# Kernel tuning notes

Measured on AMD Instinct MI355X. Metric: run time of the kernel, lower is better.

The kernel has to match this reference:

```python
import jax, jax.numpy as jnp
import numpy as np

N_NODES = 20000
N_EDGES = 320000
BATCH = 8
N_OBS = 6
N_FIXED = 10
HID = 128
N_LAYERS = 3


def setup_inputs() -> dict:
    key = jax.random.key(0)
    ks = jax.random.split(key, 6)
    x = jax.random.normal(ks[0], (BATCH * N_NODES, N_OBS), dtype=jnp.float32)
    fixed_node_features = jax.random.normal(ks[1], (N_NODES, N_FIXED), dtype=jnp.float32)
    edge_index = jax.random.randint(ks[2], (2, N_EDGES), 0, N_NODES)
    W_in = jax.random.normal(ks[3], (N_OBS + N_FIXED, HID), dtype=jnp.float32) * 0.1
    b_in = jnp.zeros((HID,), jnp.float32)
    Wg = jax.random.normal(ks[4], (N_LAYERS, HID, HID), dtype=jnp.float32) * 0.05
    bg = jnp.zeros((N_LAYERS, HID), jnp.float32)
    return {"x": x, "fixed_node_features": fixed_node_features, "W_in": W_in,
            "b_in": b_in, "Wg": Wg, "bg": bg, "edge_index": edge_index}


def reference(x, fixed_node_features, W_in, b_in, Wg, bg, edge_index):
    # GCN normalization with self-loops (PyG gcn_norm defaults):
    self_loops = jnp.arange(N_NODES)
    row = jnp.concatenate([edge_index[0], self_loops])  # source nodes [E+N]
    col = jnp.concatenate([edge_index[1], self_loops])  # target nodes [E+N]
    deg = jax.ops.segment_sum(jnp.ones_like(col, dtype=jnp.float32), col,
                              num_segments=N_NODES)
    dinv = jnp.where(deg > 0, jax.lax.rsqrt(jnp.maximum(deg, 1.0)), 0.0)
    norm = dinv[row] * dinv[col]  # [E+N]

    # input projection: [B*N, n_obs] -> [B, N, n_obs+n_fixed] -> [B, N, H]
    h = x.reshape(BATCH, N_NODES, N_OBS)
    h = jnp.concatenate(
        [h, jnp.broadcast_to(fixed_node_features, (BATCH, N_NODES, N_FIXED))],
        axis=-1)
    h = h @ W_in + b_in

    # stacked GCNConv + ReLU (gather -> normalize -> scatter-add)
    for l in range(N_LAYERS):
        t = h @ Wg[l]                              # [B, N, H]
        msgs = t[:, row, :] * norm[None, :, None]  # [B, E+N, H]
        agg = jnp.zeros_like(t).at[:, col, :].add(msgs)
        h = jax.nn.relu(agg + bg[l])

    return h.reshape(-1, HID)
```

## Files before the change

### kernel.cpp

```cpp
#include <hip/hip_runtime.h>
#include <hip/hip_bf16.h>
#include <cstdint>

#define N_NODES 20000
#define N_EDGES 320000
#define BATCH 8
#define HID 128

static constexpr size_t O_DEG  = 0;
static constexpr size_t O_CUR  = 81920;
static constexpr size_t O_OFF  = 163840;
static constexpr size_t O_DINV = 245760;
static constexpr size_t O_CSR  = 327680;
static constexpr size_t O_CSRW = 1376256;
static constexpr size_t O_HBUF = 3473408;


__global__ void count_deg(const int* __restrict__ col, int* __restrict__ deg) {
    int e = blockIdx.x * 256 + threadIdx.x;
    if (e < N_EDGES) atomicAdd(&deg[col[e]], 1);
}

__global__ void compute_dinv(const int* __restrict__ deg, float* __restrict__ dinv) {
    int i = blockIdx.x * 256 + threadIdx.x;
    if (i < N_NODES) {
        float d = (float)(deg[i] + 1);
        dinv[i] = 1.0f / sqrtf(d);
    }
}

__global__ __launch_bounds__(1024) void scan_offsets(const int* __restrict__ deg,
                                                     int* __restrict__ off) {
    __shared__ int part[1024];
    const int CH = 20;
    int tid = threadIdx.x;
    int base = tid * CH;
    int s = 0;
    for (int i = 0; i < CH; ++i) {
        int idx = base + i;
        if (idx < N_NODES) s += (deg[idx] + 7) & ~7;
    }
    part[tid] = s;
    __syncthreads();
    for (int d = 1; d < 1024; d <<= 1) {
        int add = 0;
        if (tid >= d) add = part[tid - d];
        __syncthreads();
        part[tid] += add;
        __syncthreads();
    }
    int run = part[tid] - s;
    for (int i = 0; i < CH; ++i) {
        int idx = base + i;
        if (idx < N_NODES) {
            off[idx] = run;
            run += (deg[idx] + 7) & ~7;
        }
    }
    if (tid == 1023) off[N_NODES] = part[1023];
}

__global__ void fill_csr(const int* __restrict__ rowi, const int* __restrict__ coli,
                         const float* __restrict__ dinv, const int* __restrict__ off,
                         int* __restrict__ cursor, uint16_t* __restrict__ csr,
                         float* __restrict__ csrw) {
    int e = blockIdx.x * 256 + threadIdx.x;
    if (e >= N_EDGES) return;
    int r = rowi[e], c = coli[e];
    int pos = atomicAdd(&cursor[c], 1);
    int i = off[c] + pos;
    csr[i] = (uint16_t)r;
    csrw[i] = dinv[r] * dinv[c];
}

__global__ void pad_csr(const int* __restrict__ deg, const int* __restrict__ off,
                        uint16_t* __restrict__ csr, float* __restrict__ csrw) {
    int n = blockIdx.x * 256 + threadIdx.x;
    if (n >= N_NODES) return;
    int d = deg[n];
    int pd = (d + 7) & ~7;
    int s = off[n];
    uint16_t filler = d > 0 ? csr[s + d - 1] : (uint16_t)n;
    for (int i = d; i < pd; ++i) {
        csr[s + i] = filler;
        csrw[s + i] = 0.0f;
    }
}

__global__ __launch_bounds__(64) void sort_adj(const int* __restrict__ degv,
                                               const int* __restrict__ off,
                                               uint16_t* __restrict__ csr,
                                               float* __restrict__ csrw) {
    int n = blockIdx.x;
    int s = off[n];
    int deg = degv[n];
    if (deg <= 1 || deg > 64) return;
    int l = threadIdx.x;
    int my = (l < deg) ? (int)csr[s + l] : 0x7fffffff;
    float mw = (l < deg) ? csrw[s + l] : 0.0f;
    int rank = 0;
    for (int j = 0; j < deg; ++j) {
        int kj = __shfl(my, j);
        rank += (kj < my) || (kj == my && j < l);
    }
    if (l < deg) { csr[s + rank] = (uint16_t)my; csrw[s + rank] = mw; }
}

__global__ __launch_bounds__(256) void input_proj(const float* __restrict__ x,
                                                  const float* __restrict__ fixedf,
                                                  const float* __restrict__ W,
                                                  const float* __restrict__ bvec,
                                                  float* __restrict__ h) {
    __shared__ float Ws[16 * HID];
    __shared__ float xs[BATCH * 6];
    __shared__ float fs[10];
    int n = blockIdx.x, tid = threadIdx.x;
    for (int i = tid; i < 16 * HID; i += 256) Ws[i] = W[i];
    if (tid < 48) {
        int b_ = tid / 6, o = tid % 6;
        xs[tid] = x[((size_t)b_ * N_NODES + n) * 6 + o];
    } else if (tid < 58) {
        fs[tid - 48] = fixedf[(size_t)n * 10 + (tid - 48)];
    }
    __syncthreads();
#pragma unroll
    for (int j = 0; j < 4; ++j) {
        int idx = tid + j * 256;
        int bb = idx >> 7, hh = idx & 127;
        float acc = bvec[hh];
#pragma unroll
        for (int k = 0; k < 6; ++k) acc += xs[bb * 6 + k] * Ws[k * HID + hh];
#pragma unroll
        for (int k = 0; k < 10; ++k) acc += fs[k] * Ws[(6 + k) * HID + hh];
        size_t a = ((size_t)((hh >> 5) * 8 + bb) * N_NODES + n) * 32 + (hh & 31);
        h[a] = acc;
    }
}

__global__ __launch_bounds__(256) void aggregate_xcd(const float* __restrict__ hin,
                                                     const int* __restrict__ off,
                                                     const uint16_t* __restrict__ csr,
                                                     const float* __restrict__ csrw,
                                                     const float* __restrict__ dinv,
                                                     float* __restrict__ out,
                                                     int final_scatter) {
    int bid = blockIdx.x;
    int b   = bid & 7;
    int q   = bid / 5000;
    int g   = (bid - q * 5000) >> 3;
    int tid = threadIdx.x;
    int l = tid & 63;
    int n = g * 32 + ((tid >> 6) << 3) + (l >> 3);
    int sub = l & 7;
    const size_t SB4 = (size_t)(q * 8 + b) * N_NODES * 8;

    const float4* hp4 = (const float4*)hin;
    float dn = dinv[n];
    float d2 = dn * dn;
    float4 acc = hp4[SB4 + (size_t)n * 8 + sub];
    acc.x *= d2; acc.y *= d2; acc.z *= d2; acc.w *= d2;
    float4 acc2 = make_float4(0.f, 0.f, 0.f, 0.f);

    int s = off[n], e = s + (off[n + 1] - s);
    for (int p = s; p < e; p += 8) {
        uint4  iv = *(const uint4*)(csr + p);
        float4 wa = *(const float4*)(csrw + p);
        float4 wb = *(const float4*)(csrw + p + 4);
        int s0 = iv.x & 0xffff, s1 = iv.x >> 16;
        int s2 = iv.y & 0xffff, s3 = iv.y >> 16;
        int s4 = iv.z & 0xffff, s5 = iv.z >> 16;
        int s6 = iv.w & 0xffff, s7 = iv.w >> 16;
        float4 v0 = hp4[SB4 + (size_t)s0 * 8 + sub];
        float4 v1 = hp4[SB4 + (size_t)s1 * 8 + sub];
        float4 v2 = hp4[SB4 + (size_t)s2 * 8 + sub];
        float4 v3 = hp4[SB4 + (size_t)s3 * 8 + sub];
        float4 v4 = hp4[SB4 + (size_t)s4 * 8 + sub];
        float4 v5 = hp4[SB4 + (size_t)s5 * 8 + sub];
        float4 v6 = hp4[SB4 + (size_t)s6 * 8 + sub];
        float4 v7 = hp4[SB4 + (size_t)s7 * 8 + sub];
        acc.x  += wa.x * v0.x + wa.y * v1.x + wa.z * v2.x + wa.w * v3.x;
        acc.y  += wa.x * v0.y + wa.y * v1.y + wa.z * v2.y + wa.w * v3.y;
        acc.z  += wa.x * v0.z + wa.y * v1.z + wa.z * v2.z + wa.w * v3.z;
        acc.w  += wa.x * v0.w + wa.y * v1.w + wa.z * v2.w + wa.w * v3.w;
        acc2.x += wb.x * v4.x + wb.y * v5.x + wb.z * v6.x + wb.w * v7.x;
        acc2.y += wb.x * v4.y + wb.y * v5.y + wb.z * v6.y + wb.w * v7.y;
        acc2.z += wb.x * v4.z + wb.y * v5.z + wb.z * v6.z + wb.w * v7.z;
        acc2.w += wb.x * v4.w + wb.y * v5.w + wb.z * v6.w + wb.w * v7.w;
    }
    acc.x += acc2.x; acc.y += acc2.y; acc.z += acc2.z; acc.w += acc2.w;

    size_t o4 = final_scatter ? ((size_t)(b * N_NODES + n) * 32 + q * 8 + sub)
                              : (SB4 + (size_t)n * 8 + sub);
    ((float4*)out)[o4] = acc;
}

__global__ __launch_bounds__(256) void gemm_bias_relu(const float* __restrict__ in,
                                                      float* __restrict__ outp,
                                                      const float* __restrict__ W,
                                                      const float* __restrict__ bias,
                                                      int dense) {
    __shared__ float As_T[32][132];
    __shared__ float Wls[32][HID];
    int tid = threadIdx.x;
    int rg = tid >> 4;
    int cg = tid & 15;
    int b  = blockIdx.x / 157;
    int n0 = (blockIdx.x % 157) * 128;
    float acc[8][8] = {};
    const float4* in4 = (const float4*)in;

    for (int kt = 0; kt < HID; kt += 32) {
        int q = kt >> 5;
        __syncthreads();
#pragma unroll
        for (int i = 0; i < 4; ++i) {
            int f = tid + i * 256;
            int row = f >> 3;
            int kk4 = f & 7;
            int n = n0 + row;
            if (n > N_NODES - 1) n = N_NODES - 1;
            size_t rb4 = dense ? (((size_t)b * N_NODES + n) * 32 + q * 8)
                               : (((size_t)(q * 8 + b) * N_NODES + n) * 8);
            float4 v = in4[rb4 + kk4];
            int kk = kk4 << 2;
            As_T[kk + 0][row] = v.x;
            As_T[kk + 1][row] = v.y;
            As_T[kk + 2][row] = v.z;
            As_T[kk + 3][row] = v.w;
        }
#pragma unroll
        for (int i = 0; i < 4; ++i) {
            int f = tid + i * 256;
            int row = f >> 5;
            int kk = (f & 31) << 2;
            *(float4*)&Wls[row][kk] = *(const float4*)&W[(size_t)(kt + row) * HID + kk];
        }
        __syncthreads();
#pragma unroll 8
        for (int k = 0; k < 32; ++k) {
            float4 a0 = *(const float4*)&As_T[k][rg * 8];
            float4 a1 = *(const float4*)&As_T[k][rg * 8 + 4];
            float4 w0 = *(const float4*)&Wls[k][cg * 4];
            float4 w1 = *(const float4*)&Wls[k][cg * 4 + 64];
            float av[8] = {a0.x, a0.y, a0.z, a0.w, a1.x, a1.y, a1.z, a1.w};
            float wv[8] = {w0.x, w0.y, w0.z, w0.w, w1.x, w1.y, w1.z, w1.w};
#pragma unroll
            for (int i = 0; i < 8; ++i)
#pragma unroll
                for (int j = 0; j < 8; ++j)
                    acc[i][j] += av[i] * wv[j];
        }
    }

    float4 b0 = *(const float4*)&bias[cg * 4];
    float4 b1 = *(const float4*)&bias[cg * 4 + 64];
    float4* out4 = (float4*)outp;
#pragma unroll
    for (int i = 0; i < 8; ++i) {
        int n = n0 + rg * 8 + i;
        if (n >= N_NODES) break;
        float4 o0, o1;
        o0.x = fmaxf(acc[i][0] + b0.x, 0.0f);
        o0.y = fmaxf(acc[i][1] + b0.y, 0.0f);
        o0.z = fmaxf(acc[i][2] + b0.z, 0.0f);
        o0.w = fmaxf(acc[i][3] + b0.w, 0.0f);
        o1.x = fmaxf(acc[i][4] + b1.x, 0.0f);
        o1.y = fmaxf(acc[i][5] + b1.y, 0.0f);
        o1.z = fmaxf(acc[i][6] + b1.z, 0.0f);
        o1.w = fmaxf(acc[i][7] + b1.w, 0.0f);
        if (dense) {
            size_t r4 = ((size_t)b * N_NODES + n) * 32;
            out4[r4 + cg] = o0;
            out4[r4 + cg + 16] = o1;
        } else {
            int q0 = cg >> 3, f0 = cg & 7;
            out4[((size_t)(q0 * 8 + b) * N_NODES + n) * 8 + f0] = o0;
            out4[((size_t)((q0 + 2) * 8 + b) * N_NODES + n) * 8 + f0] = o1;
        }
    }
}

extern "C" void kernel_launch(void* const* d_in, const int* in_sizes, int n_in,
                              void* d_out, int out_size, void* d_ws, size_t ws_size,
                              hipStream_t stream) {
    const float* x      = (const float*)d_in[0];
    const float* fixedf = (const float*)d_in[1];
    const float* W_in   = (const float*)d_in[2];
    const float* b_in   = (const float*)d_in[3];
    const float* Wg     = (const float*)d_in[4];
    const float* bg     = (const float*)d_in[5];
    const int*   ei     = (const int*)d_in[6];

    const int* rowi = ei;
    const int* coli = ei + N_EDGES;

    char* ws = (char*)d_ws;
    int*      deg    = (int*)(ws + O_DEG);
    int*      cursor = (int*)(ws + O_CUR);
    int*      off    = (int*)(ws + O_OFF);
    float*    dinv   = (float*)(ws + O_DINV);
    uint16_t* csr    = (uint16_t*)(ws + O_CSR);
    float*    csrw   = (float*)(ws + O_CSRW);
    float*    hA     = (float*)(ws + O_HBUF);
    float*    hB     = (float*)d_out;

    hipMemsetAsync(deg, 0, N_NODES * sizeof(int), stream);
    hipMemsetAsync(cursor, 0, N_NODES * sizeof(int), stream);

    count_deg<<<(N_EDGES + 255) / 256, 256, 0, stream>>>(coli, deg);
    compute_dinv<<<(N_NODES + 255) / 256, 256, 0, stream>>>(deg, dinv);
    scan_offsets<<<1, 1024, 0, stream>>>(deg, off);
    fill_csr<<<(N_EDGES + 255) / 256, 256, 0, stream>>>(rowi, coli, dinv, off, cursor,
                                                        csr, csrw);
    pad_csr<<<(N_NODES + 255) / 256, 256, 0, stream>>>(deg, off, csr, csrw);
    sort_adj<<<N_NODES, 64, 0, stream>>>(deg, off, csr, csrw);

    input_proj<<<N_NODES, 256, 0, stream>>>(x, fixedf, W_in, b_in, hA);

    const int AB = 4 * 5000;
    const int GB = 8 * 157;

    aggregate_xcd<<<AB, 256, 0, stream>>>(hA, off, csr, csrw, dinv, hB, 0);
    gemm_bias_relu<<<GB, 256, 0, stream>>>(hB, hB, Wg + 0 * HID * HID, bg + 0 * HID, 0);
    aggregate_xcd<<<AB, 256, 0, stream>>>(hB, off, csr, csrw, dinv, hA, 0);
    gemm_bias_relu<<<GB, 256, 0, stream>>>(hA, hA, Wg + 1 * HID * HID, bg + 1 * HID, 0);
    aggregate_xcd<<<AB, 256, 0, stream>>>(hA, off, csr, csrw, dinv, (float*)d_out, 1);
    gemm_bias_relu<<<GB, 256, 0, stream>>>((float*)d_out, (float*)d_out,
                                           Wg + 2 * HID * HID, bg + 2 * HID, 1);
}
```

Measured before the change: 591.7 us.

## Sort nodes by padded degree within groups and enlarge GEMM tiles to 256 rows

Adds a kernel that builds a per-32-node permutation sorted by padded degree, so each wavefront's 8-node slots in aggregation get similar neighbour counts and divergence drops. The GEMM kernel moves to 512 threads covering 256 node rows per block with a padded weight tile, halving the block count. The cost is an extra indirection load per node and a larger, heavier GEMM block that may reduce occupancy.

```diff
diff --git a/kernel.cpp b/kernel.cpp
--- a/kernel.cpp
+++ b/kernel.cpp
@@ -13,7 +13,8 @@
 static constexpr size_t O_DINV = 245760;
 static constexpr size_t O_CSR  = 327680;
 static constexpr size_t O_CSRW = 1376256;
-static constexpr size_t O_HBUF = 3473408;
+static constexpr size_t O_P32  = 3473408;
+static constexpr size_t O_HBUF = 3553408;
 
 
 __global__ void count_deg(const int* __restrict__ col, int* __restrict__ deg) {
@@ -106,6 +107,22 @@
     if (l < deg) { csr[s + rank] = (uint16_t)my; csrw[s + rank] = mw; }
 }
 
+__global__ __launch_bounds__(64) void build_perm32(const int* __restrict__ deg,
+                                                   int* __restrict__ perm) {
+    int tid = threadIdx.x;
+    int l = tid & 31;
+    int grp = blockIdx.x * 2 + (tid >> 5);
+    if (grp >= N_NODES / 32) return;
+    int n = grp * 32 + l;
+    int key = (deg[n] + 7) & ~7;
+    int rank = 0;
+    for (int j = 0; j < 32; ++j) {
+        int kj = __shfl(key, j, 32);
+        rank += (kj < key) || (kj == key && j < l);
+    }
+    perm[grp * 32 + rank] = n;
+}
+
 __global__ __launch_bounds__(256) void input_proj(const float* __restrict__ x,
                                                   const float* __restrict__ fixedf,
                                                   const float* __restrict__ W,
@@ -142,6 +159,7 @@
                                                      const uint16_t* __restrict__ csr,
                                                      const float* __restrict__ csrw,
                                                      const float* __restrict__ dinv,
+                                                     const int* __restrict__ perm,
                                                      float* __restrict__ out,
                                                      int final_scatter) {
     int bid = blockIdx.x;
@@ -150,7 +168,7 @@
     int g   = (bid - q * 5000) >> 3;
     int tid = threadIdx.x;
     int l = tid & 63;
-    int n = g * 32 + ((tid >> 6) << 3) + (l >> 3);
+    int n = perm[g * 32 + ((tid >> 6) << 3) + (l >> 3)];
     int sub = l & 7;
     const size_t SB4 = (size_t)(q * 8 + b) * N_NODES * 8;
 
@@ -161,7 +179,7 @@
     acc.x *= d2; acc.y *= d2; acc.z *= d2; acc.w *= d2;
     float4 acc2 = make_float4(0.f, 0.f, 0.f, 0.f);
 
-    int s = off[n], e = s + (off[n + 1] - s);
+    int s = off[n], e = off[n + 1];
     for (int p = s; p < e; p += 8) {
         uint4  iv = *(const uint4*)(csr + p);
         float4 wa = *(const float4*)(csrw + p);
@@ -194,18 +212,18 @@
     ((float4*)out)[o4] = acc;
 }
 
-__global__ __launch_bounds__(256) void gemm_bias_relu(const float* __restrict__ in,
-                                                      float* __restrict__ outp,
-                                                      const float* __restrict__ W,
-                                                      const float* __restrict__ bias,
-                                                      int dense) {
-    __shared__ float As_T[32][132];
-    __shared__ float Wls[32][HID];
+__global__ __launch_bounds__(512, 4) void gemm_bias_relu(const float* __restrict__ in,
+                                                         float* __restrict__ outp,
+                                                         const float* __restrict__ W,
+                                                         const float* __restrict__ bias,
+                                                         int dense) {
+    __shared__ float As_T[32][260];
+    __shared__ float Wls[32][132];
     int tid = threadIdx.x;
     int rg = tid >> 4;
     int cg = tid & 15;
-    int b  = blockIdx.x / 157;
-    int n0 = (blockIdx.x % 157) * 128;
+    int b  = blockIdx.x / 79;
+    int n0 = (blockIdx.x % 79) * 256;
     float acc[8][8] = {};
     const float4* in4 = (const float4*)in;
 
@@ -214,7 +232,7 @@
         __syncthreads();
 #pragma unroll
         for (int i = 0; i < 4; ++i) {
-            int f = tid + i * 256;
+            int f = tid + i * 512;
             int row = f >> 3;
             int kk4 = f & 7;
             int n = n0 + row;
@@ -229,8 +247,8 @@
             As_T[kk + 3][row] = v.w;
         }
 #pragma unroll
-        for (int i = 0; i < 4; ++i) {
-            int f = tid + i * 256;
+        for (int i = 0; i < 2; ++i) {
+            int f = tid + i * 512;
             int row = f >> 5;
             int kk = (f & 31) << 2;
             *(float4*)&Wls[row][kk] = *(const float4*)&W[(size_t)(kt + row) * HID + kk];
@@ -301,6 +319,7 @@
     float*    dinv   = (float*)(ws + O_DINV);
     uint16_t* csr    = (uint16_t*)(ws + O_CSR);
     float*    csrw   = (float*)(ws + O_CSRW);
+    int*      perm   = (int*)(ws + O_P32);
     float*    hA     = (float*)(ws + O_HBUF);
     float*    hB     = (float*)d_out;
 
@@ -314,17 +333,18 @@
                                                         csr, csrw);
     pad_csr<<<(N_NODES + 255) / 256, 256, 0, stream>>>(deg, off, csr, csrw);
     sort_adj<<<N_NODES, 64, 0, stream>>>(deg, off, csr, csrw);
+    build_perm32<<<(N_NODES / 32 + 1) / 2, 64, 0, stream>>>(deg, perm);
 
     input_proj<<<N_NODES, 256, 0, stream>>>(x, fixedf, W_in, b_in, hA);
 
     const int AB = 4 * 5000;
-    const int GB = 8 * 157;
-
-    aggregate_xcd<<<AB, 256, 0, stream>>>(hA, off, csr, csrw, dinv, hB, 0);
-    gemm_bias_relu<<<GB, 256, 0, stream>>>(hB, hB, Wg + 0 * HID * HID, bg + 0 * HID, 0);
-    aggregate_xcd<<<AB, 256, 0, stream>>>(hB, off, csr, csrw, dinv, hA, 0);
-    gemm_bias_relu<<<GB, 256, 0, stream>>>(hA, hA, Wg + 1 * HID * HID, bg + 1 * HID, 0);
-    aggregate_xcd<<<AB, 256, 0, stream>>>(hA, off, csr, csrw, dinv, (float*)d_out, 1);
-    gemm_bias_relu<<<GB, 256, 0, stream>>>((float*)d_out, (float*)d_out,
+    const int GB = 8 * 79;
+
+    aggregate_xcd<<<AB, 256, 0, stream>>>(hA, off, csr, csrw, dinv, perm, hB, 0);
+    gemm_bias_relu<<<GB, 512, 0, stream>>>(hB, hB, Wg + 0 * HID * HID, bg + 0 * HID, 0);
+    aggregate_xcd<<<AB, 256, 0, stream>>>(hB, off, csr, csrw, dinv, perm, hA, 0);
+    gemm_bias_relu<<<GB, 512, 0, stream>>>(hA, hA, Wg + 1 * HID * HID, bg + 1 * HID, 0);
+    aggregate_xcd<<<AB, 256, 0, stream>>>(hA, off, csr, csrw, dinv, perm, (float*)d_out, 1);
+    gemm_bias_relu<<<GB, 512, 0, stream>>>((float*)d_out, (float*)d_out,
                                            Wg + 2 * HID * HID, bg + 2 * HID, 1);
 }
```

After: 627.8 us. +6.1%, slower.
